# Performance work log

Measured on AMD Instinct MI355X. Metric: run time of the kernel, lower is better.

## Reference

```python
import jax, jax.numpy as jnp
import numpy as np

N_NODES = 100000
N_EDGES = 1600000
N_GRAPHS = 2048
BN_EPS = 1e-5


def _bn(h, gamma, beta):
    # BatchNorm1d in training mode: biased batch stats over the node axis
    mean = jnp.mean(h, axis=0)
    var = jnp.var(h, axis=0)
    return gamma * (h - mean) * jax.lax.rsqrt(var + BN_EPS) + beta


def _gin_layer(x, src, dst, w1, b1, gamma, beta, w2, b2):
    # GINConv with eps=0: mlp(x + sum_{j->i} x_j)
    agg = jax.ops.segment_sum(x[src], dst, num_segments=N_NODES)
    h = agg + x
    h = h @ w1 + b1
    h = jax.nn.relu(_bn(h, gamma, beta))
    h = h @ w2 + b2
    return jax.nn.relu(h)  # outer F.relu after GINConv (dropout = identity in eval)


def setup_inputs() -> dict:
    key = jax.random.key(0)
    ks = jax.random.split(key, 24)
    d = {}
    d['x'] = jax.random.normal(ks[0], (N_NODES, 66), dtype=jnp.float32)
    d['edge_index'] = jax.random.randint(ks[1], (2, N_EDGES), 0, N_NODES, dtype=jnp.int64)
    d['batch'] = jnp.sort(jax.random.randint(ks[2], (N_NODES,), 0, N_GRAPHS, dtype=jnp.int64))
    dims = [(66, 128), (128, 256), (256, 128)]
    ki = 3
    for li, (din, dout) in enumerate(dims):
        s1 = 1.0 / np.sqrt(din)
        s2 = 1.0 / np.sqrt(dout)
        d[f'g{li}_w1'] = jax.random.uniform(ks[ki + 0], (din, dout), jnp.float32, -s1, s1)
        d[f'g{li}_b1'] = jax.random.uniform(ks[ki + 1], (dout,), jnp.float32, -s1, s1)
        d[f'g{li}_gamma'] = jnp.ones((dout,), jnp.float32)
        d[f'g{li}_beta'] = jnp.zeros((dout,), jnp.float32)
        d[f'g{li}_w2'] = jax.random.uniform(ks[ki + 2], (dout, dout), jnp.float32, -s2, s2)
        d[f'g{li}_b2'] = jax.random.uniform(ks[ki + 3], (dout,), jnp.float32, -s2, s2)
        ki += 4
    fcd = [(128, 1024), (1024, 128)]
    for li, (din, dout) in enumerate(fcd):
        s = 1.0 / np.sqrt(din)
        d[f'fc{li}_w'] = jax.random.uniform(ks[ki + 0], (din, dout), jnp.float32, -s, s)
        d[f'fc{li}_b'] = jax.random.uniform(ks[ki + 1], (dout,), jnp.float32, -s, s)
        ki += 2
    return d


def reference(x, edge_index, batch,
              g0_w1, g0_b1, g0_gamma, g0_beta, g0_w2, g0_b2,
              g1_w1, g1_b1, g1_gamma, g1_beta, g1_w2, g1_b2,
              g2_w1, g2_b1, g2_gamma, g2_beta, g2_w2, g2_b2,
              fc0_w, fc0_b, fc1_w, fc1_b):
    src, dst = edge_index[0], edge_index[1]
    h = _gin_layer(x, src, dst, g0_w1, g0_b1, g0_gamma, g0_beta, g0_w2, g0_b2)
    h = _gin_layer(h, src, dst, g1_w1, g1_b1, g1_gamma, g1_beta, g1_w2, g1_b2)
    h = _gin_layer(h, src, dst, g2_w1, g2_b1, g2_gamma, g2_beta, g2_w2, g2_b2)
    # global_add_pool over graphs
    g = jax.ops.segment_sum(h, batch, num_segments=N_GRAPHS)
    g = jax.nn.relu(g @ fc0_w + fc0_b)
    return g @ fc1_w + fc1_b
```

## Files before the change

### kernel.cpp

```cpp
#include <hip/hip_runtime.h>

#define NNODES 100000
#define NEDGES 1600000
#define NGRAPHS 2048
#define BN_EPS 1e-5f

typedef __attribute__((ext_vector_type(8))) short bf16x8;
typedef __attribute__((ext_vector_type(4))) float f32x4;

__device__ __forceinline__ short f2bf(float x) {
    unsigned u = __float_as_uint(x);
    unsigned r = u + 0x7FFF + ((u >> 16) & 1);
    return (short)(r >> 16);
}
__device__ __forceinline__ float bf2f(short h) {
    return __uint_as_float(((unsigned)(unsigned short)h) << 16);
}

__global__ __launch_bounds__(256) void degoff_kernel(const int* __restrict__ dstA,
                                                     int* __restrict__ degp,
                                                     int* __restrict__ off) {
    int e = blockIdx.x * 256 + threadIdx.x;
    if (e < NEDGES) {
        int d = dstA[e];
        int c = atomicAdd(&degp[d << 4], 1);
        off[e] = (d << 8) | c;
    }
}

__global__ __launch_bounds__(256) void scan1_kernel(const int* __restrict__ degp,
                                                    int* __restrict__ partials) {
    int b = blockIdx.x;
    int i = b * 256 + threadIdx.x;
    int v = (i < NNODES) ? degp[i << 4] : 0;
    __shared__ int wsum[4];
#pragma unroll
    for (int off = 32; off; off >>= 1) v += __shfl_down(v, off);
    if ((threadIdx.x & 63) == 0) wsum[threadIdx.x >> 6] = v;
    __syncthreads();
    if (threadIdx.x == 0) partials[b] = wsum[0] + wsum[1] + wsum[2] + wsum[3];
}

__global__ __launch_bounds__(512) void scan2_kernel(int* __restrict__ partials, int nb) {
    __shared__ int s[512];
    int t = threadIdx.x;
    int v = (t < nb) ? partials[t] : 0;
    s[t] = v;
    __syncthreads();
    for (int off = 1; off < 512; off <<= 1) {
        int u = (t >= off) ? s[t - off] : 0;
        __syncthreads();
        s[t] += u;
        __syncthreads();
    }
    if (t < nb) partials[t] = s[t] - v;
}

__global__ __launch_bounds__(256) void scan3_kernel(const int* __restrict__ degp,
                                                    const int* __restrict__ partials,
                                                    int* __restrict__ rowptr,
                                                    const int* __restrict__ batch,
                                                    int* __restrict__ gstart) {
    int b = blockIdx.x;
    int t = threadIdx.x;
    int i = b * 256 + t;
    __shared__ int s[256];
    int v = (i < NNODES) ? degp[i << 4] : 0;
    s[t] = v;
    __syncthreads();
    for (int off = 1; off < 256; off <<= 1) {
        int u = (t >= off) ? s[t - off] : 0;
        __syncthreads();
        s[t] += u;
        __syncthreads();
    }
    if (i < NNODES) {
        int ex = partials[b] + s[t] - v;
        rowptr[i] = ex;
        int bb = batch[i];
        int bp = (i == 0) ? -1 : batch[i - 1];
        for (int g = bp + 1; g <= bb; ++g) gstart[g] = i;
        if (i == NNODES - 1)
            for (int g = bb + 1; g <= NGRAPHS; ++g) gstart[g] = NNODES;
    }
    if (b == 0 && t == 0) rowptr[NNODES] = NEDGES;
}

__global__ __launch_bounds__(256) void fill2_kernel(const int* __restrict__ srcA,
                                                    const int* __restrict__ rowptr,
                                                    const int* __restrict__ off,
                                                    int* __restrict__ adj) {
    int e = blockIdx.x * 256 + threadIdx.x;
    if (e < NEDGES) {
        int v = off[e];
        adj[rowptr[v >> 8] + (v & 255)] = srcA[e];
    }
}

template <int DIM, int CHUNK, int OSTRIDE, bool SPLIT>
__global__ __launch_bounds__(256) void gather_kernel(const float* __restrict__ x,
                                                     const int* __restrict__ rowptr,
                                                     const int* __restrict__ adj,
                                                     float* __restrict__ agg,
                                                     short* __restrict__ oh,
                                                     short* __restrict__ ol,
                                                     const float* __restrict__ bias) {
    constexpr int PE = DIM / CHUNK;
    constexpr int PEL = SPLIT ? (OSTRIDE / CHUNK) : PE;
    int gid = blockIdx.x * 256 + threadIdx.x;
    if (gid >= NNODES * PEL) return;
    int node = gid / PEL;
    int c = gid - node * PEL;
    if constexpr (SPLIT) {
        if (c >= PE) {
            size_t o = (size_t)node * OSTRIDE + c * CHUNK;
            if constexpr (CHUNK == 4) {
                short4 z;
                z.x = z.y = z.z = z.w = 0;
                *(short4*)&oh[o] = z;
                *(short4*)&ol[o] = z;
            } else {
                short2 z;
                z.x = z.y = 0;
                *(short2*)&oh[o] = z;
                *(short2*)&ol[o] = z;
            }
            return;
        }
    }
    const int beg = rowptr[node];
    const int end = rowptr[node + 1];
    if constexpr (CHUNK == 4) {
        const float4* xp = (const float4*)x;
        float4 acc = xp[(size_t)node * PE + c];
        float4 acc1 = make_float4(0.f, 0.f, 0.f, 0.f);
        int i = beg;
        for (; i + 8 <= end; i += 8) {
            int s0 = adj[i + 0], s1 = adj[i + 1], s2 = adj[i + 2], s3 = adj[i + 3];
            int s4 = adj[i + 4], s5 = adj[i + 5], s6 = adj[i + 6], s7 = adj[i + 7];
            float4 v0 = xp[(size_t)s0 * PE + c];
            float4 v1 = xp[(size_t)s1 * PE + c];
            float4 v2 = xp[(size_t)s2 * PE + c];
            float4 v3 = xp[(size_t)s3 * PE + c];
            float4 v4 = xp[(size_t)s4 * PE + c];
            float4 v5 = xp[(size_t)s5 * PE + c];
            float4 v6 = xp[(size_t)s6 * PE + c];
            float4 v7 = xp[(size_t)s7 * PE + c];
            acc.x += v0.x + v1.x; acc.y += v0.y + v1.y; acc.z += v0.z + v1.z; acc.w += v0.w + v1.w;
            acc1.x += v2.x + v3.x; acc1.y += v2.y + v3.y; acc1.z += v2.z + v3.z; acc1.w += v2.w + v3.w;
            acc.x += v4.x + v5.x; acc.y += v4.y + v5.y; acc.z += v4.z + v5.z; acc.w += v4.w + v5.w;
            acc1.x += v6.x + v7.x; acc1.y += v6.y + v7.y; acc1.z += v6.z + v7.z; acc1.w += v6.w + v7.w;
        }
        for (; i + 4 <= end; i += 4) {
            int s0 = adj[i + 0], s1 = adj[i + 1], s2 = adj[i + 2], s3 = adj[i + 3];
            float4 v0 = xp[(size_t)s0 * PE + c];
            float4 v1 = xp[(size_t)s1 * PE + c];
            float4 v2 = xp[(size_t)s2 * PE + c];
            float4 v3 = xp[(size_t)s3 * PE + c];
            acc.x += v0.x + v1.x; acc.y += v0.y + v1.y; acc.z += v0.z + v1.z; acc.w += v0.w + v1.w;
            acc1.x += v2.x + v3.x; acc1.y += v2.y + v3.y; acc1.z += v2.z + v3.z; acc1.w += v2.w + v3.w;
        }
        for (; i < end; ++i) {
            int s = adj[i];
            float4 v = xp[(size_t)s * PE + c];
            acc.x += v.x; acc.y += v.y; acc.z += v.z; acc.w += v.w;
        }
        acc.x += acc1.x; acc.y += acc1.y; acc.z += acc1.z; acc.w += acc1.w;
        if (bias) {
            float4 b = *(const float4*)&bias[c * 4];
            acc.x += b.x; acc.y += b.y; acc.z += b.z; acc.w += b.w;
        }
        if constexpr (SPLIT) {
            size_t o = (size_t)node * OSTRIDE + c * 4;
            short4 h4, l4;
            h4.x = f2bf(acc.x); l4.x = f2bf(acc.x - bf2f(h4.x));
            h4.y = f2bf(acc.y); l4.y = f2bf(acc.y - bf2f(h4.y));
            h4.z = f2bf(acc.z); l4.z = f2bf(acc.z - bf2f(h4.z));
            h4.w = f2bf(acc.w); l4.w = f2bf(acc.w - bf2f(h4.w));
            *(short4*)&oh[o] = h4;
            *(short4*)&ol[o] = l4;
        } else {
            *(float4*)&agg[(size_t)node * OSTRIDE + c * 4] = acc;
        }
    } else {
        const float2* xp = (const float2*)x;
        float2 acc = xp[(size_t)node * PE + c];
        float2 acc1 = make_float2(0.f, 0.f);
        int i = beg;
        for (; i + 8 <= end; i += 8) {
            int s0 = adj[i + 0], s1 = adj[i + 1], s2 = adj[i + 2], s3 = adj[i + 3];
            int s4 = adj[i + 4], s5 = adj[i + 5], s6 = adj[i + 6], s7 = adj[i + 7];
            float2 v0 = xp[(size_t)s0 * PE + c];
            float2 v1 = xp[(size_t)s1 * PE + c];
            float2 v2 = xp[(size_t)s2 * PE + c];
            float2 v3 = xp[(size_t)s3 * PE + c];
            float2 v4 = xp[(size_t)s4 * PE + c];
            float2 v5 = xp[(size_t)s5 * PE + c];
            float2 v6 = xp[(size_t)s6 * PE + c];
            float2 v7 = xp[(size_t)s7 * PE + c];
            acc.x += v0.x + v1.x; acc.y += v0.y + v1.y;
            acc1.x += v2.x + v3.x; acc1.y += v2.y + v3.y;
            acc.x += v4.x + v5.x; acc.y += v4.y + v5.y;
            acc1.x += v6.x + v7.x; acc1.y += v6.y + v7.y;
        }
        for (; i + 4 <= end; i += 4) {
            int s0 = adj[i + 0], s1 = adj[i + 1], s2 = adj[i + 2], s3 = adj[i + 3];
            float2 v0 = xp[(size_t)s0 * PE + c];
            float2 v1 = xp[(size_t)s1 * PE + c];
            float2 v2 = xp[(size_t)s2 * PE + c];
            float2 v3 = xp[(size_t)s3 * PE + c];
            acc.x += v0.x + v1.x; acc.y += v0.y + v1.y;
            acc1.x += v2.x + v3.x; acc1.y += v2.y + v3.y;
        }
        for (; i < end; ++i) {
            int s = adj[i];
            float2 v = xp[(size_t)s * PE + c];
            acc.x += v.x; acc.y += v.y;
        }
        acc.x += acc1.x; acc.y += acc1.y;
        if constexpr (SPLIT) {
            size_t o = (size_t)node * OSTRIDE + c * 2;
            short2 h2, l2;
            h2.x = f2bf(acc.x); l2.x = f2bf(acc.x - bf2f(h2.x));
            h2.y = f2bf(acc.y); l2.y = f2bf(acc.y - bf2f(h2.y));
            *(short2*)&oh[o] = h2;
            *(short2*)&ol[o] = l2;
        } else {
            *(float2*)&agg[(size_t)node * OSTRIDE + c * 2] = acc;
        }
    }
}

template <int N>
__global__ __launch_bounds__(256) void bnstats_kernel(const float* __restrict__ h,
                                                      float* __restrict__ sums) {
    constexpr int SHIFT = (N == 128) ? 7 : 8;
    int t = blockIdx.x * 256 + threadIdx.x;
    int col = t & (N - 1);
    int slice = t >> SHIFT;
    int stride = (gridDim.x * 256) >> SHIFT;
    float s = 0.f, s2 = 0.f;
    for (int r = slice; r < NNODES; r += stride) {
        float v = h[(size_t)r * N + col];
        s += v;
        s2 += v * v;
    }
    atomicAdd(&sums[col], s);
    atomicAdd(&sums[256 + col], s2);
}

__global__ void bnfinal_kernel(float* __restrict__ sums, const float* __restrict__ gamma,
                               const float* __restrict__ beta, float* __restrict__ scsh, int N,
                               float invM) {
    int c = threadIdx.x;
    if (c < N) {
        float mean = sums[c] * invM;
        float var = sums[256 + c] * invM - mean * mean;
        float sc = gamma[c] * rsqrtf(var + BN_EPS);
        scsh[c] = sc;
        scsh[256 + c] = beta[c] - mean * sc;
    }
    sums[c] = 0.f;
    sums[256 + c] = 0.f;
}

struct WDesc {
    const float* W;
    int Kw, N, KT, hioff, looff;
};
struct WDescs {
    WDesc d[8];
    int cum[9];
};
__global__ __launch_bounds__(256) void wprep_all_kernel(WDescs wd, short* __restrict__ wf) {
    int idx = blockIdx.x * 256 + threadIdx.x;
    if (idx >= wd.cum[8]) return;
    int s = 0;
#pragma unroll
    for (int i = 1; i < 8; ++i) s += (idx >= wd.cum[i]);
    int r = idx - wd.cum[s];
    const WDesc D = wd.d[s];
    int j = r & 7;
    int lane = (r >> 3) & 63;
    int t = r >> 9;
    int kt = t % D.KT;
    int nt = t / D.KT;
    int k = kt * 32 + ((lane >> 4) << 3) + j;
    int n = (nt << 4) + (lane & 15);
    float w = (k < D.Kw) ? D.W[(size_t)k * D.N + n] : 0.f;
    short hi = f2bf(w);
    wf[D.hioff + r] = hi;
    wf[D.looff + r] = f2bf(w - bf2f(hi));
}

template <int NT, int KTLOOP, int KTT, int MROWS, bool BNRELU_A, bool RELU_OUT, bool FUSE_STATS,
          bool SPLITK, bool ASPLIT, bool SPLIT_OUT, int MINW>
__global__ __launch_bounds__(256, MINW) void gemm_mfma_kernel(
    const float* __restrict__ A, const short* __restrict__ Ah, const short* __restrict__ Al,
    const short* __restrict__ whi, const short* __restrict__ wlo, const float* __restrict__ bias,
    const float* __restrict__ scsh, float* __restrict__ C, short* __restrict__ Ch,
    short* __restrict__ Cl, float* __restrict__ stats, int M, int Kst, int N) {
    __shared__ float sstat[512];
    const int tid = threadIdx.x;
    const int wave = tid >> 6;
    const int lane = tid & 63;
    const int quad = lane >> 4;
    const int l16 = lane & 15;
    const int mrow = blockIdx.x * (64 * MROWS) + wave * 16 + l16;
    const int ngrp = blockIdx.y * NT * 16;
    const size_t wgrp = (size_t)blockIdx.y * NT * KTT * 512;
    const int ktbeg = SPLITK ? blockIdx.z * KTLOOP : 0;
    float* Cb = SPLITK ? C + (size_t)blockIdx.z * M * N : C;

    if (FUSE_STATS) {
        sstat[tid] = 0.f;
        sstat[tid + 256] = 0.f;
        __syncthreads();
    }

    f32x4 acc[MROWS][NT] = {};

    auto kstep = [&](int kt) {
        const int kq = kt * 32 + quad * 8;
        bf16x8 ahi[MROWS], alo[MROWS];
        if constexpr (ASPLIT) {
#pragma unroll
            for (int m = 0; m < MROWS; ++m) {
                const size_t ro = (size_t)(mrow + m * 64) * Kst + kq;
                ahi[m] = *(const bf16x8*)(Ah + ro);
                alo[m] = *(const bf16x8*)(Al + ro);
            }
        } else {
            float sc[8], sh[8];
            if constexpr (BNRELU_A) {
                float4 sc0 = *(const float4*)&scsh[kq];
                float4 sc1 = *(const float4*)&scsh[kq + 4];
                float4 sh0 = *(const float4*)&scsh[256 + kq];
                float4 sh1 = *(const float4*)&scsh[256 + kq + 4];
                sc[0] = sc0.x; sc[1] = sc0.y; sc[2] = sc0.z; sc[3] = sc0.w;
                sc[4] = sc1.x; sc[5] = sc1.y; sc[6] = sc1.z; sc[7] = sc1.w;
                sh[0] = sh0.x; sh[1] = sh0.y; sh[2] = sh0.z; sh[3] = sh0.w;
                sh[4] = sh1.x; sh[5] = sh1.y; sh[6] = sh1.z; sh[7] = sh1.w;
            }
#pragma unroll
            for (int m = 0; m < MROWS; ++m) {
                const float* ap = A + (size_t)(mrow + m * 64) * Kst + kq;
                float4 x0 = *(const float4*)ap;
                float4 x1 = *(const float4*)(ap + 4);
                float a8[8] = {x0.x, x0.y, x0.z, x0.w, x1.x, x1.y, x1.z, x1.w};
                if constexpr (BNRELU_A) {
#pragma unroll
                    for (int i = 0; i < 8; ++i) a8[i] = fmaxf(a8[i] * sc[i] + sh[i], 0.f);
                }
#pragma unroll
                for (int i = 0; i < 8; ++i) {
                    short h = f2bf(a8[i]);
                    ahi[m][i] = h;
                    alo[m][i] = f2bf(a8[i] - bf2f(h));
                }
            }
        }
#pragma unroll
        for (int nt = 0; nt < NT; ++nt) {
            const size_t boff = wgrp + (((size_t)nt * KTT + kt) << 9) + ((size_t)lane << 3);
            bf16x8 bh = *(const bf16x8*)(whi + boff);
            bf16x8 bl = *(const bf16x8*)(wlo + boff);
#pragma unroll
            for (int m = 0; m < MROWS; ++m) {
                acc[m][nt] = __builtin_amdgcn_mfma_f32_16x16x32_bf16(ahi[m], bh, acc[m][nt], 0, 0, 0);
                acc[m][nt] = __builtin_amdgcn_mfma_f32_16x16x32_bf16(alo[m], bh, acc[m][nt], 0, 0, 0);
                acc[m][nt] = __builtin_amdgcn_mfma_f32_16x16x32_bf16(ahi[m], bl, acc[m][nt], 0, 0, 0);
                acc[m][nt] = __builtin_amdgcn_mfma_f32_16x16x32_bf16(alo[m], bl, acc[m][nt], 0, 0, 0);
            }
        }
    };

    if constexpr (ASPLIT) {
#pragma unroll 2
        for (int k = 0; k < KTLOOP; ++k) kstep(ktbeg + k);
    } else {
#pragma unroll 1
        for (int k = 0; k < KTLOOP; ++k) kstep(ktbeg + k);
    }

#pragma unroll
    for (int m = 0; m < MROWS; ++m) {
        const int mbase = blockIdx.x * (64 * MROWS) + m * 64 + wave * 16 + quad * 4;
#pragma unroll
        for (int nt = 0; nt < NT; ++nt) {
            int gn = ngrp + nt * 16 + l16;
            float bv = bias ? bias[gn] : 0.f;
            float s = 0.f, s2 = 0.f;
#pragma unroll
            for (int r = 0; r < 4; ++r) {
                int gm = mbase + r;
                float v = acc[m][nt][r] + bv;
                if (RELU_OUT) v = fmaxf(v, 0.f);
                if (gm < M) {
                    if constexpr (SPLIT_OUT) {
                        short h = f2bf(v);
                        Ch[(size_t)gm * N + gn] = h;
                        Cl[(size_t)gm * N + gn] = f2bf(v - bf2f(h));
                    } else {
                        Cb[(size_t)gm * N + gn] = v;
                    }
                    if (FUSE_STATS) {
                        s += v;
                        s2 += v * v;
                    }
                }
            }
            if (FUSE_STATS) {
                s += __shfl_xor(s, 16);
                s += __shfl_xor(s, 32);
                s2 += __shfl_xor(s2, 16);
                s2 += __shfl_xor(s2, 32);
                if (quad == 0) {
                    atomicAdd(&sstat[gn], s);
                    atomicAdd(&sstat[256 + gn], s2);
                }
            }
        }
    }
    if (FUSE_STATS) {
        __syncthreads();
        if (tid < N) {
            atomicAdd(&stats[tid], sstat[tid]);
            atomicAdd(&stats[256 + tid], sstat[256 + tid]);
        }
    }
}

__global__ __launch_bounds__(256) void splitk_reduce_kernel(const float* __restrict__ part,
                                                            const float* __restrict__ bias,
                                                            float* __restrict__ out) {
    const int i4 = blockIdx.x * 256 + threadIdx.x;
    const int TOT4 = NGRAPHS * 128 / 4;
    if (i4 >= TOT4) return;
    const float4* p = (const float4*)part;
    float4 acc = make_float4(0.f, 0.f, 0.f, 0.f);
#pragma unroll
    for (int c = 0; c < 8; ++c) {
        float4 v = p[(size_t)c * TOT4 + i4];
        acc.x += v.x;
        acc.y += v.y;
        acc.z += v.z;
        acc.w += v.w;
    }
    float4 b = ((const float4*)bias)[i4 & 31];
    acc.x += b.x;
    acc.y += b.y;
    acc.z += b.z;
    acc.w += b.w;
    ((float4*)out)[i4] = acc;
}

template <bool SPLIT>
__global__ __launch_bounds__(128) void pool_seg_kernel(const float* __restrict__ h,
                                                       const int* __restrict__ gstart,
                                                       float* __restrict__ g,
                                                       short* __restrict__ oh,
                                                       short* __restrict__ ol) {
    int gr = blockIdx.x;
    int t = threadIdx.x;
    int beg = gstart[gr];
    int end = gstart[gr + 1];
    float acc = 0.f;
    for (int r = beg; r < end; ++r) acc += h[(size_t)r * 128 + t];
    if constexpr (SPLIT) {
        short hh = f2bf(acc);
        oh[(size_t)gr * 128 + t] = hh;
        ol[(size_t)gr * 128 + t] = f2bf(acc - bf2f(hh));
    } else {
        g[(size_t)gr * 128 + t] = acc;
    }
}

extern "C" void kernel_launch(void* const* d_in, const int* in_sizes, int n_in, void* d_out,
                              int out_size, void* d_ws, size_t ws_size, hipStream_t stream) {
    const float* x = (const float*)d_in[0];
    const int* ei = (const int*)d_in[1];
    const int* batch = (const int*)d_in[2];
    const int* srcA = ei;
    const int* dstA = ei + NEDGES;

    const float* g0_w1 = (const float*)d_in[3];
    const float* g0_b1 = (const float*)d_in[4];
    const float* g0_ga = (const float*)d_in[5];
    const float* g0_be = (const float*)d_in[6];
    const float* g0_w2 = (const float*)d_in[7];
    const float* g0_b2 = (const float*)d_in[8];
    const float* g1_w1 = (const float*)d_in[9];
    const float* g1_b1 = (const float*)d_in[10];
    const float* g1_ga = (const float*)d_in[11];
    const float* g1_be = (const float*)d_in[12];
    const float* g1_w2 = (const float*)d_in[13];
    const float* g1_b2 = (const float*)d_in[14];
    const float* g2_w1 = (const float*)d_in[15];
    const float* g2_b1 = (const float*)d_in[16];
    const float* g2_ga = (const float*)d_in[17];
    const float* g2_be = (const float*)d_in[18];
    const float* g2_w2 = (const float*)d_in[19];
    const float* g2_b2 = (const float*)d_in[20];
    const float* fc0_w = (const float*)d_in[21];
    const float* fc0_b = (const float*)d_in[22];
    const float* fc1_w = (const float*)d_in[23];
    const float* fc1_b = (const float*)d_in[24];

    float* ws = (float*)d_ws;
    const size_t BUF = (size_t)NNODES * 256;
    float* R0 = ws;
    float* R1 = R0 + BUF;
    float* stats = R1 + BUF;
    float* scsh = stats + 512;
    float* g = scsh + 512;
    float* gh = g + (size_t)NGRAPHS * 128;
    int* rowptr = (int*)(gh + (size_t)NGRAPHS * 1024);
    int* adj = rowptr + NNODES + 4;
    int* partials = adj + NEDGES;
    int* gstart = partials + 512;
    short* wf = (short*)(gstart + 2052);

    int* degp = (int*)R0;
    int* off = degp + NNODES * 16;

    short* whi[8];
    short* wlo[8];
    for (int i = 0; i < 6; ++i) {
        whi[i] = wf + (size_t)i * 131072;
        wlo[i] = whi[i] + 65536;
    }
    whi[6] = wf + 6 * 131072;
    wlo[6] = whi[6] + 131072;
    whi[7] = whi[6] + 262144;
    wlo[7] = whi[7] + 131072;

    short* P0h = (short*)R0;
    short* P0l = P0h + (size_t)NNODES * 96;
    short* P1h = (short*)R1;
    short* P1l = P1h + (size_t)NNODES * 128;
    short* P2h = (short*)R1;
    short* P2l = P2h + (size_t)NNODES * 256;
    short* GPh = (short*)g;
    short* GPl = GPh + (size_t)NGRAPHS * 128;
    short* GHh = (short*)gh;
    short* GHl = GHh + (size_t)NGRAPHS * 1024;

    const int GB = (NNODES + 63) / 64;
    const int GB2 = (NNODES + 127) / 128;
    const int NB = (NNODES + 255) / 256;
    const int EB = (NEDGES + 255) / 256;
    (void)GB;

    hipMemsetAsync(degp, 0, (size_t)NNODES * 16 * sizeof(int), stream);
    hipMemsetAsync(stats, 0, 512 * sizeof(float), stream);
    degoff_kernel<<<EB, 256, 0, stream>>>(dstA, degp, off);
    scan1_kernel<<<NB, 256, 0, stream>>>(degp, partials);
    scan2_kernel<<<1, 512, 0, stream>>>(partials, NB);
    scan3_kernel<<<NB, 256, 0, stream>>>(degp, partials, rowptr, batch, gstart);
    fill2_kernel<<<EB, 256, 0, stream>>>(srcA, rowptr, off, adj);

    {
        WDescs wd;
        const float* Wp[8] = {g0_w1, g0_w2, g1_w1, g1_w2, g2_w1, g2_w2, fc0_w, fc1_w};
        const int Kw[8] = {66, 128, 128, 256, 256, 128, 128, 1024};
        const int Nn[8] = {128, 128, 256, 256, 128, 128, 1024, 128};
        const int KT[8] = {3, 4, 4, 8, 8, 4, 4, 32};
        int cum = 0;
        wd.cum[0] = 0;
        for (int i = 0; i < 8; ++i) {
            wd.d[i].W = Wp[i];
            wd.d[i].Kw = Kw[i];
            wd.d[i].N = Nn[i];
            wd.d[i].KT = KT[i];
            wd.d[i].hioff = (int)(whi[i] - wf);
            wd.d[i].looff = (int)(wlo[i] - wf);
            cum += (Nn[i] >> 4) * KT[i] * 512;
            wd.cum[i + 1] = cum;
        }
        wprep_all_kernel<<<(wd.cum[8] + 255) / 256, 256, 0, stream>>>(wd, wf);
    }

    gather_kernel<66, 2, 96, true><<<(NNODES * 48 + 255) / 256, 256, 0, stream>>>(
        x, rowptr, adj, nullptr, P0h, P0l, nullptr);
    gemm_mfma_kernel<8, 3, 3, 2, false, false, true, false, true, false, 3>
        <<<GB2, 256, 0, stream>>>(nullptr, P0h, P0l, whi[0], wlo[0], g0_b1, nullptr, R1, nullptr,
                                  nullptr, stats, NNODES, 96, 128);
    bnfinal_kernel<<<1, 256, 0, stream>>>(stats, g0_ga, g0_be, scsh, 128, 1.0f / NNODES);
    gemm_mfma_kernel<8, 4, 4, 2, true, true, false, false, false, false, 3>
        <<<GB2, 256, 0, stream>>>(R1, nullptr, nullptr, whi[1], wlo[1], g0_b2, scsh, R0, nullptr,
                                  nullptr, nullptr, NNODES, 128, 128);

    gather_kernel<128, 4, 128, true><<<(NNODES * 32 + 255) / 256, 256, 0, stream>>>(
        R0, rowptr, adj, nullptr, P1h, P1l, nullptr);
    gemm_mfma_kernel<8, 4, 4, 2, false, false, true, false, true, false, 3>
        <<<dim3(GB2, 2), 256, 0, stream>>>(nullptr, P1h, P1l, whi[2], wlo[2], g1_b1, nullptr, R0,
                                           nullptr, nullptr, stats, NNODES, 128, 256);
    bnfinal_kernel<<<1, 256, 0, stream>>>(stats, g1_ga, g1_be, scsh, 256, 1.0f / NNODES);
    gemm_mfma_kernel<8, 8, 8, 2, true, true, false, false, false, true, 3>
        <<<dim3(GB2, 2), 256, 0, stream>>>(R0, nullptr, nullptr, whi[3], wlo[3], g1_b2, scsh,
                                           nullptr, P2h, P2l, nullptr, NNODES, 256, 256);

    gemm_mfma_kernel<8, 8, 8, 2, false, false, false, false, true, false, 3>
        <<<GB2, 256, 0, stream>>>(nullptr, P2h, P2l, whi[4], wlo[4], nullptr, nullptr, R0, nullptr,
                                  nullptr, nullptr, NNODES, 256, 128);
    gather_kernel<128, 4, 128, false><<<(NNODES * 32 + 255) / 256, 256, 0, stream>>>(
        R0, rowptr, adj, R1, nullptr, nullptr, g2_b1);
    bnstats_kernel<128><<<256, 256, 0, stream>>>(R1, stats);
    bnfinal_kernel<<<1, 256, 0, stream>>>(stats, g2_ga, g2_be, scsh, 128, 1.0f / NNODES);
    gemm_mfma_kernel<8, 4, 4, 2, true, true, false, false, false, false, 3>
        <<<GB2, 256, 0, stream>>>(R1, nullptr, nullptr, whi[5], wlo[5], g2_b2, scsh, R0, nullptr,
                                  nullptr, nullptr, NNODES, 128, 128);

    pool_seg_kernel<true><<<NGRAPHS, 128, 0, stream>>>(R0, gstart, nullptr, GPh, GPl);

    gemm_mfma_kernel<8, 4, 4, 2, false, true, false, false, true, true, 3>
        <<<dim3(NGRAPHS / 128, 8), 256, 0, stream>>>(nullptr, GPh, GPl, whi[6], wlo[6], fc0_b,
                                                     nullptr, nullptr, GHh, GHl, nullptr, NGRAPHS,
                                                     128, 1024);
    gemm_mfma_kernel<8, 4, 32, 2, false, false, false, true, true, false, 3>
        <<<dim3(NGRAPHS / 128, 1, 8), 256, 0, stream>>>(nullptr, GHh, GHl, whi[7], wlo[7], nullptr,
                                                        nullptr, R1, nullptr, nullptr, nullptr,
                                                        NGRAPHS, 1024, 128);
    splitk_reduce_kernel<<<(NGRAPHS * 128 / 4 + 255) / 256, 256, 0, stream>>>(R1, fc1_b,
                                                                              (float*)d_out);
}
```

Measured before the change: 1.110 ms.

## Pad input features to 68 for float4 gather and enlarge GEMM row tiles

Adds a kernel that copies the 66-wide input features into a 68-wide padded buffer, so the first-layer gather can use 4-float chunks instead of 2-float chunks and halve its thread count. It also changes three bf16-split GEMM launches from 128-row to 192-row blocks (a tile parameter from 2 to 3) and lowers another template parameter from 3 to 2, likely a pipeline stage or occupancy setting. The padding pass adds an extra read and write of the input array, and the larger tiles raise register and LDS use per block.

```diff
diff --git a/kernel.cpp b/kernel.cpp
--- a/kernel.cpp
+++ b/kernel.cpp
@@ -95,6 +95,24 @@
         int v = off[e];
         adj[rowptr[v >> 8] + (v & 255)] = srcA[e];
     }
+}
+
+__global__ __launch_bounds__(256) void pad66_kernel(const float* __restrict__ x,
+                                                    float* __restrict__ xpad) {
+    int idx = blockIdx.x * 256 + threadIdx.x;
+    if (idx >= NNODES * 17) return;
+    int node = idx / 17;
+    int c = idx - node * 17;
+    float4 v;
+    if (c < 16) {
+        float2 a = *(const float2*)&x[(size_t)node * 66 + c * 4];
+        float2 b = *(const float2*)&x[(size_t)node * 66 + c * 4 + 2];
+        v = make_float4(a.x, a.y, b.x, b.y);
+    } else {
+        float2 a = *(const float2*)&x[(size_t)node * 66 + 64];
+        v = make_float4(a.x, a.y, 0.f, 0.f);
+    }
+    *(float4*)&xpad[(size_t)node * 68 + c * 4] = v;
 }
 
 template <int DIM, int CHUNK, int OSTRIDE, bool SPLIT>
@@ -523,6 +541,7 @@
 
     int* degp = (int*)R0;
     int* off = degp + NNODES * 16;
+    float* xpad = R1;
 
     short* whi[8];
     short* wlo[8];
@@ -546,14 +565,14 @@
     short* GHh = (short*)gh;
     short* GHl = GHh + (size_t)NGRAPHS * 1024;
 
-    const int GB = (NNODES + 63) / 64;
     const int GB2 = (NNODES + 127) / 128;
+    const int GB3 = (NNODES + 191) / 192;
     const int NB = (NNODES + 255) / 256;
     const int EB = (NEDGES + 255) / 256;
-    (void)GB;
 
     hipMemsetAsync(degp, 0, (size_t)NNODES * 16 * sizeof(int), stream);
     hipMemsetAsync(stats, 0, 512 * sizeof(float), stream);
+    pad66_kernel<<<(NNODES * 17 + 255) / 256, 256, 0, stream>>>(x, xpad);
     degoff_kernel<<<EB, 256, 0, stream>>>(dstA, degp, off);
     scan1_kernel<<<NB, 256, 0, stream>>>(degp, partials);
     scan2_kernel<<<1, 512, 0, stream>>>(partials, NB);
@@ -581,10 +600,10 @@
         wprep_all_kernel<<<(wd.cum[8] + 255) / 256, 256, 0, stream>>>(wd, wf);
     }
 
-    gather_kernel<66, 2, 96, true><<<(NNODES * 48 + 255) / 256, 256, 0, stream>>>(
-        x, rowptr, adj, nullptr, P0h, P0l, nullptr);
-    gemm_mfma_kernel<8, 3, 3, 2, false, false, true, false, true, false, 3>
-        <<<GB2, 256, 0, stream>>>(nullptr, P0h, P0l, whi[0], wlo[0], g0_b1, nullptr, R1, nullptr,
+    gather_kernel<68, 4, 96, true><<<(NNODES * 24 + 255) / 256, 256, 0, stream>>>(
+        xpad, rowptr, adj, nullptr, P0h, P0l, nullptr);
+    gemm_mfma_kernel<8, 3, 3, 3, false, false, true, false, true, false, 2>
+        <<<GB3, 256, 0, stream>>>(nullptr, P0h, P0l, whi[0], wlo[0], g0_b1, nullptr, R1, nullptr,
                                   nullptr, stats, NNODES, 96, 128);
     bnfinal_kernel<<<1, 256, 0, stream>>>(stats, g0_ga, g0_be, scsh, 128, 1.0f / NNODES);
     gemm_mfma_kernel<8, 4, 4, 2, true, true, false, false, false, false, 3>
@@ -593,16 +612,16 @@
 
     gather_kernel<128, 4, 128, true><<<(NNODES * 32 + 255) / 256, 256, 0, stream>>>(
         R0, rowptr, adj, nullptr, P1h, P1l, nullptr);
-    gemm_mfma_kernel<8, 4, 4, 2, false, false, true, false, true, false, 3>
-        <<<dim3(GB2, 2), 256, 0, stream>>>(nullptr, P1h, P1l, whi[2], wlo[2], g1_b1, nullptr, R0,
+    gemm_mfma_kernel<8, 4, 4, 3, false, false, true, false, true, false, 2>
+        <<<dim3(GB3, 2), 256, 0, stream>>>(nullptr, P1h, P1l, whi[2], wlo[2], g1_b1, nullptr, R0,
                                            nullptr, nullptr, stats, NNODES, 128, 256);
     bnfinal_kernel<<<1, 256, 0, stream>>>(stats, g1_ga, g1_be, scsh, 256, 1.0f / NNODES);
     gemm_mfma_kernel<8, 8, 8, 2, true, true, false, false, false, true, 3>
         <<<dim3(GB2, 2), 256, 0, stream>>>(R0, nullptr, nullptr, whi[3], wlo[3], g1_b2, scsh,
                                            nullptr, P2h, P2l, nullptr, NNODES, 256, 256);
 
-    gemm_mfma_kernel<8, 8, 8, 2, false, false, false, false, true, false, 3>
-        <<<GB2, 256, 0, stream>>>(nullptr, P2h, P2l, whi[4], wlo[4], nullptr, nullptr, R0, nullptr,
+    gemm_mfma_kernel<8, 8, 8, 3, false, false, false, false, true, false, 2>
+        <<<GB3, 256, 0, stream>>>(nullptr, P2h, P2l, whi[4], wlo[4], nullptr, nullptr, R0, nullptr,
                                   nullptr, nullptr, NNODES, 256, 128);
     gather_kernel<128, 4, 128, false><<<(NNODES * 32 + 255) / 256, 256, 0, stream>>>(
         R0, rowptr, adj, R1, nullptr, nullptr, g2_b1);
```

New measurement: 1.134 ms. +2.1%, slower.
